# Performance work log

Measured on AMD Instinct MI355X. Metric: run time of the kernel, lower is better.

The kernel has to match this reference:

```python
import jax, jax.numpy as jnp
import numpy as np

B, T, C = 4, 2048, 768
H = 12  # n_head; head_dim = C // H = 64


def setup_inputs() -> dict:
    key = jax.random.key(0)
    k1, k2, k3, k4, k5 = jax.random.split(key, 5)
    scale = 0.02
    return {
        "x": jax.random.normal(k1, (B, T, C), dtype=jnp.float32),
        "w_attn": jax.random.normal(k2, (C, 3 * C), dtype=jnp.float32) * scale,
        "b_attn": jax.random.normal(k3, (3 * C,), dtype=jnp.float32) * scale,
        "w_proj": jax.random.normal(k4, (C, C), dtype=jnp.float32) * scale,
        "b_proj": jax.random.normal(k5, (C,), dtype=jnp.float32) * scale,
    }


def reference(x, w_attn, b_attn, w_proj, b_proj):
    Bx, Tx, Cx = x.shape
    hd = Cx // H  # head dim
    qkv = x @ w_attn + b_attn                       # [B, T, 3C]
    q, k, v = jnp.split(qkv, 3, axis=2)
    # [B, T, H, hd] -> [B, H, T, hd]
    q = q.reshape(Bx, Tx, H, hd).transpose(0, 2, 1, 3)
    k = k.reshape(Bx, Tx, H, hd).transpose(0, 2, 1, 3)
    v = v.reshape(Bx, Tx, H, hd).transpose(0, 2, 1, 3)
    att = jnp.einsum('bhqd,bhkd->bhqk', q, k) / jnp.sqrt(jnp.float32(hd))
    causal = jnp.tril(jnp.ones((Tx, Tx), dtype=bool))
    att = jnp.where(causal[None, None, :, :], att, -jnp.inf)
    att = jax.nn.softmax(att, axis=-1)
    y = jnp.einsum('bhqk,bhkd->bhqd', att, v)       # [B, H, T, hd]
    y = y.transpose(0, 2, 1, 3).reshape(Bx, Tx, Cx)
    return y @ w_proj + b_proj
```

## Files before the change

### kernel.cpp

```cpp
#include <hip/hip_runtime.h>
#include <hip/hip_bf16.h>

using f32x4 = __attribute__((ext_vector_type(4))) float;
using s16x8 = __attribute__((ext_vector_type(8))) short;

#define MFMA16x16x32(a, b, c) __builtin_amdgcn_mfma_f32_16x16x32_bf16((a), (b), (c), 0, 0, 0)

#define AS_G(p) ((const __attribute__((address_space(1))) void*)(p))
#define AS_L(p) ((__attribute__((address_space(3))) void*)(p))

#define BARRIER_LGKM() do { \
    asm volatile("s_waitcnt lgkmcnt(0)" ::: "memory"); \
    __builtin_amdgcn_s_barrier(); \
} while (0)

static __device__ __forceinline__ unsigned short f2bf(float f) {
    unsigned int u = __float_as_uint(f);
    u = (u + 0x7fffu + ((u >> 16) & 1u)) >> 16;
    return (unsigned short)u;
}
static __device__ __forceinline__ unsigned int cvt_pk_bf2(float lo, float hi) {
    unsigned int r;
    asm("v_cvt_pk_bf16_f32 %0, %1, %2" : "=v"(r) : "v"(lo), "v"(hi));
    return r;
}
static __device__ __forceinline__ int swz128(int r, int c) { return (r * 128 + c) ^ ((r & 7) << 4); }

__global__ __launch_bounds__(256)
void prologue_kernel(const float* __restrict__ x, unsigned short* __restrict__ xb,
                     const float* __restrict__ w_attn, unsigned short* __restrict__ wTa,
                     const float* __restrict__ w_proj, unsigned short* __restrict__ wTp) {
    __shared__ float tile[32][33];
    const int bid = blockIdx.x, tid = threadIdx.x;
    if (bid < 2048) {
        const int n = 8192 * 768;
        int i = (bid * 256 + tid) * 4;
        const int stride = 2048 * 256 * 4;
        for (; i < n; i += stride) {
            float4 v = *(const float4*)(x + i);
            ushort4 o;
            o.x = f2bf(v.x); o.y = f2bf(v.y); o.z = f2bf(v.z); o.w = f2bf(v.w);
            *(ushort4*)(xb + i) = o;
        }
    } else {
        const float* w; unsigned short* wt; int K, N, bx, by;
        if (bid < 3776) {
            int id = bid - 2048; w = w_attn; wt = wTa; K = 768; N = 2304;
            bx = id % 72; by = id / 72;
        } else {
            int id = bid - 3776; w = w_proj; wt = wTp; K = 768; N = 768;
            bx = id % 24; by = id / 24;
        }
        const int tx = tid & 31, ty = tid >> 5;
        const int n0 = bx * 32, k0 = by * 32;
#pragma unroll
        for (int r = 0; r < 4; r++)
            tile[ty * 4 + r][tx] = w[(size_t)(k0 + ty * 4 + r) * N + n0 + tx];
        __syncthreads();
#pragma unroll
        for (int r = 0; r < 4; r++)
            wt[(size_t)(n0 + ty * 4 + r) * K + k0 + tx] = f2bf(tile[tx][ty * 4 + r]);
    }
}

template <bool OUT_BF16>
__global__ __launch_bounds__(256, 3)
void gemm_bt64(const unsigned short* __restrict__ A, const unsigned short* __restrict__ Bt,
               const float* __restrict__ bias, void* __restrict__ Cout,
               unsigned short* __restrict__ Vt,
               int M, int N, int K, int ldc, int qcols, float qscale) {
    __shared__ char smem[49152];
    const int tid = threadIdx.x, wid = tid >> 6, lane = tid & 63;
    const int g = lane >> 4, lr = lane & 15;
    const int nx = N >> 7;
    const int ypx = (M >> 6) >> 3;
    const int xcd = blockIdx.x & 7, ii = blockIdx.x >> 3;
    const int m0 = (xcd * ypx + ii / nx) * 64;
    const int n0 = (ii % nx) * 128;

    f32x4 acc[4][2];
#pragma unroll
    for (int i = 0; i < 4; i++)
#pragma unroll
        for (int j = 0; j < 2; j++) acc[i][j] = f32x4{0.f, 0.f, 0.f, 0.f};

    const int rbase = lane >> 3;
    const int cSw = ((lane & 7) << 4) ^ (rbase << 4);

    auto STAGE = [&](int buf, int kt) {
        char* base = smem + buf * 24576;
#pragma unroll
        for (int ww = 0; ww < 2; ww++) {
            int w = wid * 2 + ww;
            int r = w * 8 + rbase;
            const unsigned short* srcA = A + (size_t)(m0 + r) * K + kt + (cSw >> 1);
            __builtin_amdgcn_global_load_lds(AS_G(srcA), AS_L(base + w * 1024), 16, 0, 0);
        }
#pragma unroll
        for (int ww = 0; ww < 4; ww++) {
            int w = wid * 4 + ww;
            int r = w * 8 + rbase;
            const unsigned short* srcB = Bt + (size_t)(n0 + r) * K + kt + (cSw >> 1);
            __builtin_amdgcn_global_load_lds(AS_G(srcB), AS_L(base + 8192 + w * 1024), 16, 0, 0);
        }
    };

    const int nk = K >> 6;
    STAGE(0, 0);

    for (int t = 0; t < nk; t++) {
        if (t + 1 < nk) {
            STAGE((t + 1) & 1, (t + 1) << 6);
            asm volatile("s_waitcnt vmcnt(6)" ::: "memory");
        } else {
            asm volatile("s_waitcnt vmcnt(0)" ::: "memory");
        }
        __builtin_amdgcn_s_barrier();
        char* cbase = smem + (t & 1) * 24576;
#pragma unroll
        for (int ks = 0; ks < 2; ks++) {
            s16x8 af[4], bfr[2];
#pragma unroll
            for (int i = 0; i < 4; i++)
                af[i] = *(const s16x8*)(cbase + swz128(i * 16 + lr, ks * 64 + g * 16));
#pragma unroll
            for (int j = 0; j < 2; j++)
                bfr[j] = *(const s16x8*)(cbase + 8192 + swz128(wid * 32 + j * 16 + lr, ks * 64 + g * 16));
#pragma unroll
            for (int i = 0; i < 4; i++)
#pragma unroll
                for (int j = 0; j < 2; j++)
                    acc[i][j] = MFMA16x16x32(af[i], bfr[j], acc[i][j]);
        }
        BARRIER_LGKM();
    }

    if (Vt != nullptr && n0 >= 1536) {
#pragma unroll
        for (int j = 0; j < 2; j++) {
            int dl = wid * 32 + j * 16 + lr;
            float bv = bias[n0 + dl];
#pragma unroll
            for (int i = 0; i < 4; i++) {
                int tl = i * 16 + g * 4;
                ushort4 o4;
                o4.x = f2bf(acc[i][j][0] + bv);
                o4.y = f2bf(acc[i][j][1] + bv);
                o4.z = f2bf(acc[i][j][2] + bv);
                o4.w = f2bf(acc[i][j][3] + bv);
                *(ushort4*)(smem + swz128(dl, tl * 2)) = o4;
            }
        }
        __syncthreads();
        const int bb = m0 >> 11, t0 = m0 & 2047;
#pragma unroll
        for (int it = 0; it < 4; it++) {
            int dl = it * 32 + (tid >> 3);
            int dg = (n0 - 1536) + dl;
            int hh = dg >> 6, dd = dg & 63;
            s16x8 v = *(const s16x8*)(smem + swz128(dl, (tid & 7) * 16));
            *(s16x8*)(Vt + ((((size_t)bb * 12 + hh) * 64 + dd) << 11) + t0 + (tid & 7) * 8) = v;
        }
    } else {
#pragma unroll
        for (int j = 0; j < 2; j++) {
            int c = n0 + wid * 32 + j * 16 + lr;
            float bv = bias[c];
            float cscale = (c < qcols) ? qscale : 1.0f;
#pragma unroll
            for (int i = 0; i < 4; i++) {
#pragma unroll
                for (int rg = 0; rg < 4; rg++) {
                    int r = m0 + i * 16 + g * 4 + rg;
                    float val = (acc[i][j][rg] + bv) * cscale;
                    if constexpr (OUT_BF16)
                        ((unsigned short*)Cout)[(size_t)r * ldc + c] = f2bf(val);
                    else
                        ((float*)Cout)[(size_t)r * ldc + c] = val;
                }
            }
        }
    }
}

__global__ __launch_bounds__(256, 2)
void attn_kernel(const unsigned short* __restrict__ qk, const unsigned short* __restrict__ Vt,
                 unsigned short* __restrict__ y) {
    __shared__ char smem[49152];
    const int tid = threadIdx.x, wid = tid >> 6, lane = tid & 63;
    const int g = lane >> 4, lr = lane & 15;
    const int T = 2048;

    const int s = blockIdx.x;
    const int xcd = s & 7, i = s >> 3;
    const int grp = xcd * 6 + (i >> 4);
    const int qpi = i & 15;
    const int h = grp % 12, b = grp / 12;
    const int qtA = qpi, qtB = 31 - qpi;
    const int q0A = qtA * 64, q0B = qtB * 64;

    s16x8 vone;
#pragma unroll
    for (int e = 0; e < 8; e++) vone[e] = (short)0x3F80;

    const unsigned short* qrowA = qk + (size_t)(b * T + q0A + wid * 16 + lr) * 1536 + h * 64;
    const unsigned short* qrowB = qk + (size_t)(b * T + q0B + wid * 16 + lr) * 1536 + h * 64;
    s16x8 aqA[2], aqB[2];
    aqA[0] = *(const s16x8*)(qrowA + g * 8);
    aqA[1] = *(const s16x8*)(qrowA + 32 + g * 8);
    aqB[0] = *(const s16x8*)(qrowB + g * 8);
    aqB[1] = *(const s16x8*)(qrowB + 32 + g * 8);

    f32x4 oA[4], oB[4], lsumA, lsumB;
#pragma unroll
    for (int r = 0; r < 4; r++) { oA[r] = f32x4{0.f, 0.f, 0.f, 0.f}; oB[r] = f32x4{0.f, 0.f, 0.f, 0.f}; }
    lsumA = f32x4{0.f, 0.f, 0.f, 0.f};
    lsumB = f32x4{0.f, 0.f, 0.f, 0.f};

    const int rbase = lane >> 3;
    const int cSw = ((lane & 7) << 4) ^ (rbase << 4);
    const unsigned short* pkBase = qk + (size_t)(b * T) * 1536 + 768 + h * 64 + (cSw >> 1);
    const unsigned short* pvBase = Vt + (((size_t)b * 12 + h) << 17) + (cSw >> 1);

    auto STAGE = [&](int buf, int j0) {
        char* kb = smem + buf * 8192;
        char* vb = smem + 16384 + buf * 8192;
#pragma unroll
        for (int ww = 0; ww < 2; ww++) {
            int w = wid * 2 + ww;
            int jj = w * 8 + rbase;
            const unsigned short* srcK = pkBase + (size_t)(j0 + jj) * 1536;
            __builtin_amdgcn_global_load_lds(AS_G(srcK), AS_L(kb + w * 1024), 16, 0, 0);
            const unsigned short* srcV = pvBase + ((size_t)jj << 11) + j0;
            __builtin_amdgcn_global_load_lds(AS_G(srcV), AS_L(vb + w * 1024), 16, 0, 0);
        }
    };

    const int ntA = qtA + 1, ntB = qtB + 1;

    STAGE(0, 0);

    char* const pbaseB = smem + 32768 + wid * 2048;
    char* const pbaseA = smem + 40960 + wid * 2048;
    const int q_rel = wid * 16 + lr;

    for (int t = 0; t < ntB; t++) {
        asm volatile("s_waitcnt vmcnt(0)" ::: "memory");
        BARRIER_LGKM();
        if (t + 1 < ntB) STAGE((t + 1) & 1, (t + 1) * 64);

        char* kbase = smem + (t & 1) * 8192;
        char* vbase = smem + 16384 + (t & 1) * 8192;
        const bool actA = (t < ntA);

        {
            f32x4 st[4];
            __builtin_amdgcn_s_setprio(1);
#pragma unroll
            for (int nf = 0; nf < 4; nf++) {
                f32x4 sf = f32x4{0.f, 0.f, 0.f, 0.f};
#pragma unroll
                for (int ks = 0; ks < 2; ks++) {
                    s16x8 ak = *(const s16x8*)(kbase + swz128(nf * 16 + lr, (ks * 32 + g * 8) * 2));
                    sf = MFMA16x16x32(ak, aqB[ks], sf);
                }
                st[nf] = sf;
            }
            __builtin_amdgcn_s_setprio(0);
            const bool diag = (t == ntB - 1);
#pragma unroll
            for (int nf = 0; nf < 4; nf++)
#pragma unroll
                for (int rg = 0; rg < 4; rg++) {
                    float p = __builtin_amdgcn_exp2f(st[nf][rg]);
                    if (diag && (nf * 16 + g * 4 + rg > q_rel)) p = 0.f;
                    st[nf][rg] = p;
                }
#pragma unroll
            for (int nf = 0; nf < 4; nf++) {
                uint2 dw;
                dw.x = cvt_pk_bf2(st[nf][0], st[nf][1]);
                dw.y = cvt_pk_bf2(st[nf][2], st[nf][3]);
                *(uint2*)(pbaseB + swz128(lr, nf * 32 + g * 8)) = dw;
            }
        }
        if (actA) {
            f32x4 st[4];
            __builtin_amdgcn_s_setprio(1);
#pragma unroll
            for (int nf = 0; nf < 4; nf++) {
                f32x4 sf = f32x4{0.f, 0.f, 0.f, 0.f};
#pragma unroll
                for (int ks = 0; ks < 2; ks++) {
                    s16x8 ak = *(const s16x8*)(kbase + swz128(nf * 16 + lr, (ks * 32 + g * 8) * 2));
                    sf = MFMA16x16x32(ak, aqA[ks], sf);
                }
                st[nf] = sf;
            }
            __builtin_amdgcn_s_setprio(0);
            const bool diag = (t == ntA - 1);
#pragma unroll
            for (int nf = 0; nf < 4; nf++)
#pragma unroll
                for (int rg = 0; rg < 4; rg++) {
                    float p = __builtin_amdgcn_exp2f(st[nf][rg]);
                    if (diag && (nf * 16 + g * 4 + rg > q_rel)) p = 0.f;
                    st[nf][rg] = p;
                }
#pragma unroll
            for (int nf = 0; nf < 4; nf++) {
                uint2 dw;
                dw.x = cvt_pk_bf2(st[nf][0], st[nf][1]);
                dw.y = cvt_pk_bf2(st[nf][2], st[nf][3]);
                *(uint2*)(pbaseA + swz128(lr, nf * 32 + g * 8)) = dw;
            }
        }

        {
            s16x8 pf[2];
#pragma unroll
            for (int ks = 0; ks < 2; ks++)
                pf[ks] = *(const s16x8*)(pbaseB + swz128(lr, ks * 64 + g * 16));
            __builtin_amdgcn_s_setprio(1);
#pragma unroll
            for (int nf = 0; nf < 4; nf++) {
#pragma unroll
                for (int ks = 0; ks < 2; ks++) {
                    s16x8 bv = *(const s16x8*)(vbase + swz128(nf * 16 + lr, ks * 64 + g * 16));
                    oB[nf] = MFMA16x16x32(pf[ks], bv, oB[nf]);
                }
            }
            lsumB = MFMA16x16x32(pf[0], vone, lsumB);
            lsumB = MFMA16x16x32(pf[1], vone, lsumB);
            __builtin_amdgcn_s_setprio(0);
        }
        if (actA) {
            s16x8 pf[2];
#pragma unroll
            for (int ks = 0; ks < 2; ks++)
                pf[ks] = *(const s16x8*)(pbaseA + swz128(lr, ks * 64 + g * 16));
            __builtin_amdgcn_s_setprio(1);
#pragma unroll
            for (int nf = 0; nf < 4; nf++) {
#pragma unroll
                for (int ks = 0; ks < 2; ks++) {
                    s16x8 bv = *(const s16x8*)(vbase + swz128(nf * 16 + lr, ks * 64 + g * 16));
                    oA[nf] = MFMA16x16x32(pf[ks], bv, oA[nf]);
                }
            }
            lsumA = MFMA16x16x32(pf[0], vone, lsumA);
            lsumA = MFMA16x16x32(pf[1], vone, lsumA);
            __builtin_amdgcn_s_setprio(0);
        }
    }

#pragma unroll
    for (int which = 0; which < 2; which++) {
        const f32x4 lsum = which ? lsumB : lsumA;
        const int q0 = which ? q0B : q0A;
        f32x4* o = which ? oB : oA;
        float linv_q[4];
#pragma unroll
        for (int rg = 0; rg < 4; rg++) linv_q[rg] = 1.0f / lsum[rg];
#pragma unroll
        for (int nf = 0; nf < 4; nf++) {
#pragma unroll
            for (int rg = 0; rg < 4; rg++) {
                int row = b * T + q0 + wid * 16 + g * 4 + rg;
                int col = h * 64 + nf * 16 + lr;
                y[(size_t)row * 768 + col] = f2bf(o[nf][rg] * linv_q[rg]);
            }
        }
    }
}

extern "C" void kernel_launch(void* const* d_in, const int* in_sizes, int n_in,
                              void* d_out, int out_size, void* d_ws, size_t ws_size,
                              hipStream_t stream) {
    const float* x      = (const float*)d_in[0];
    const float* w_attn = (const float*)d_in[1];
    const float* b_attn = (const float*)d_in[2];
    const float* w_proj = (const float*)d_in[3];
    const float* b_proj = (const float*)d_in[4];

    char* ws = (char*)d_ws;
    unsigned short* qk  = (unsigned short*)(ws);
    unsigned short* Vt  = (unsigned short*)(ws + 25165824);
    unsigned short* wTa = (unsigned short*)(ws + 37748736);
    unsigned short* wTp = (unsigned short*)(ws + 41287680);

    const bool big = ws_size >= (size_t)55050240;
    unsigned short* xb = (unsigned short*)d_out;
    unsigned short* yb = big ? (unsigned short*)(ws + 42467328)
                             : (unsigned short*)((char*)d_out + 12582912);
    float* projOut = big ? (float*)d_out : (float*)ws;

    prologue_kernel<<<4352, 256, 0, stream>>>(x, xb, w_attn, wTa, w_proj, wTp);

    gemm_bt64<true><<<2304, 256, 0, stream>>>(xb, wTa, b_attn, (void*)qk, Vt,
                                              8192, 2304, 768, 1536, 768, 0.1803368801111244f);
    attn_kernel<<<768, 256, 0, stream>>>(qk, Vt, yb);
    gemm_bt64<false><<<768, 256, 0, stream>>>(yb, wTp, b_proj, (void*)projOut, nullptr,
                                              8192, 768, 768, 768, 0, 1.0f);
    if (!big)
        hipMemcpyAsync(d_out, projOut, 25165824, hipMemcpyDeviceToDevice, stream);
}
```

Before: 115.4 us.

## Process paired query tiles sequentially instead of sharing K/V tiles

The attention kernel stops processing its two causal query tiles (qpi and 31-qpi) together over one shared K/V stream. It now runs them one after another, each with its own K/V staging loop, which frees one P buffer and cuts LDS from 48KB to 40KB. The cost is that K/V tiles for the shorter range are loaded twice, and a barrier separates the two passes. Barriers also drop the explicit lgkmcnt(0) wait, which relies on the compiler's own waitcnt insertion for LDS reads.

```diff
diff --git a/kernel.cpp b/kernel.cpp
--- a/kernel.cpp
+++ b/kernel.cpp
@@ -8,11 +8,6 @@
 
 #define AS_G(p) ((const __attribute__((address_space(1))) void*)(p))
 #define AS_L(p) ((__attribute__((address_space(3))) void*)(p))
-
-#define BARRIER_LGKM() do { \
-    asm volatile("s_waitcnt lgkmcnt(0)" ::: "memory"); \
-    __builtin_amdgcn_s_barrier(); \
-} while (0)
 
 static __device__ __forceinline__ unsigned short f2bf(float f) {
     unsigned int u = __float_as_uint(f);
@@ -132,7 +127,7 @@
                 for (int j = 0; j < 2; j++)
                     acc[i][j] = MFMA16x16x32(af[i], bfr[j], acc[i][j]);
         }
-        BARRIER_LGKM();
+        __builtin_amdgcn_s_barrier();
     }
 
     if (Vt != nullptr && n0 >= 1536) {
@@ -186,7 +181,7 @@
 __global__ __launch_bounds__(256, 2)
 void attn_kernel(const unsigned short* __restrict__ qk, const unsigned short* __restrict__ Vt,
                  unsigned short* __restrict__ y) {
-    __shared__ char smem[49152];
+    __shared__ char smem[40960];
     const int tid = threadIdx.x, wid = tid >> 6, lane = tid & 63;
     const int g = lane >> 4, lr = lane & 15;
     const int T = 2048;
@@ -196,26 +191,10 @@
     const int grp = xcd * 6 + (i >> 4);
     const int qpi = i & 15;
     const int h = grp % 12, b = grp / 12;
-    const int qtA = qpi, qtB = 31 - qpi;
-    const int q0A = qtA * 64, q0B = qtB * 64;
 
     s16x8 vone;
 #pragma unroll
     for (int e = 0; e < 8; e++) vone[e] = (short)0x3F80;
-
-    const unsigned short* qrowA = qk + (size_t)(b * T + q0A + wid * 16 + lr) * 1536 + h * 64;
-    const unsigned short* qrowB = qk + (size_t)(b * T + q0B + wid * 16 + lr) * 1536 + h * 64;
-    s16x8 aqA[2], aqB[2];
-    aqA[0] = *(const s16x8*)(qrowA + g * 8);
-    aqA[1] = *(const s16x8*)(qrowA + 32 + g * 8);
-    aqB[0] = *(const s16x8*)(qrowB + g * 8);
-    aqB[1] = *(const s16x8*)(qrowB + 32 + g * 8);
-
-    f32x4 oA[4], oB[4], lsumA, lsumB;
-#pragma unroll
-    for (int r = 0; r < 4; r++) { oA[r] = f32x4{0.f, 0.f, 0.f, 0.f}; oB[r] = f32x4{0.f, 0.f, 0.f, 0.f}; }
-    lsumA = f32x4{0.f, 0.f, 0.f, 0.f};
-    lsumB = f32x4{0.f, 0.f, 0.f, 0.f};
 
     const int rbase = lane >> 3;
     const int cSw = ((lane & 7) << 4) ^ (rbase << 4);
@@ -236,24 +215,35 @@
         }
     };
 
-    const int ntA = qtA + 1, ntB = qtB + 1;
-
-    STAGE(0, 0);
-
-    char* const pbaseB = smem + 32768 + wid * 2048;
-    char* const pbaseA = smem + 40960 + wid * 2048;
+    char* const pbase = smem + 32768 + wid * 2048;
     const int q_rel = wid * 16 + lr;
 
-    for (int t = 0; t < ntB; t++) {
-        asm volatile("s_waitcnt vmcnt(0)" ::: "memory");
-        BARRIER_LGKM();
-        if (t + 1 < ntB) STAGE((t + 1) & 1, (t + 1) * 64);
-
-        char* kbase = smem + (t & 1) * 8192;
-        char* vbase = smem + 16384 + (t & 1) * 8192;
-        const bool actA = (t < ntA);
-
-        {
+    for (int pp = 0; pp < 2; pp++) {
+        const int qt = pp ? (31 - qpi) : qpi;
+        const int q0 = qt * 64;
+        const int nt = qt + 1;
+
+        const unsigned short* qrow = qk + (size_t)(b * T + q0 + wid * 16 + lr) * 1536 + h * 64;
+        s16x8 aq[2];
+        aq[0] = *(const s16x8*)(qrow + g * 8);
+        aq[1] = *(const s16x8*)(qrow + 32 + g * 8);
+
+        f32x4 o[4], lsum;
+#pragma unroll
+        for (int r = 0; r < 4; r++) o[r] = f32x4{0.f, 0.f, 0.f, 0.f};
+        lsum = f32x4{0.f, 0.f, 0.f, 0.f};
+
+        if (pp) __builtin_amdgcn_s_barrier();
+        STAGE(0, 0);
+
+        for (int t = 0; t < nt; t++) {
+            asm volatile("s_waitcnt vmcnt(0)" ::: "memory");
+            __builtin_amdgcn_s_barrier();
+            if (t + 1 < nt) STAGE((t + 1) & 1, (t + 1) * 64);
+
+            char* kbase = smem + (t & 1) * 8192;
+            char* vbase = smem + 16384 + (t & 1) * 8192;
+
             f32x4 st[4];
             __builtin_amdgcn_s_setprio(1);
 #pragma unroll
@@ -262,12 +252,13 @@
 #pragma unroll
                 for (int ks = 0; ks < 2; ks++) {
                     s16x8 ak = *(const s16x8*)(kbase + swz128(nf * 16 + lr, (ks * 32 + g * 8) * 2));
-                    sf = MFMA16x16x32(ak, aqB[ks], sf);
+                    sf = MFMA16x16x32(ak, aq[ks], sf);
                 }
                 st[nf] = sf;
             }
             __builtin_amdgcn_s_setprio(0);
-            const bool diag = (t == ntB - 1);
+
+            const bool diag = (t == nt - 1);
 #pragma unroll
             for (int nf = 0; nf < 4; nf++)
 #pragma unroll
@@ -281,84 +272,27 @@
                 uint2 dw;
                 dw.x = cvt_pk_bf2(st[nf][0], st[nf][1]);
                 dw.y = cvt_pk_bf2(st[nf][2], st[nf][3]);
-                *(uint2*)(pbaseB + swz128(lr, nf * 32 + g * 8)) = dw;
-            }
-        }
-        if (actA) {
-            f32x4 st[4];
-            __builtin_amdgcn_s_setprio(1);
-#pragma unroll
-            for (int nf = 0; nf < 4; nf++) {
-                f32x4 sf = f32x4{0.f, 0.f, 0.f, 0.f};
-#pragma unroll
-                for (int ks = 0; ks < 2; ks++) {
-                    s16x8 ak = *(const s16x8*)(kbase + swz128(nf * 16 + lr, (ks * 32 + g * 8) * 2));
-                    sf = MFMA16x16x32(ak, aqA[ks], sf);
-                }
-                st[nf] = sf;
-            }
-            __builtin_amdgcn_s_setprio(0);
-            const bool diag = (t == ntA - 1);
-#pragma unroll
-            for (int nf = 0; nf < 4; nf++)
-#pragma unroll
-                for (int rg = 0; rg < 4; rg++) {
-                    float p = __builtin_amdgcn_exp2f(st[nf][rg]);
-                    if (diag && (nf * 16 + g * 4 + rg > q_rel)) p = 0.f;
-                    st[nf][rg] = p;
-                }
-#pragma unroll
-            for (int nf = 0; nf < 4; nf++) {
-                uint2 dw;
-                dw.x = cvt_pk_bf2(st[nf][0], st[nf][1]);
-                dw.y = cvt_pk_bf2(st[nf][2], st[nf][3]);
-                *(uint2*)(pbaseA + swz128(lr, nf * 32 + g * 8)) = dw;
-            }
-        }
-
-        {
+                *(uint2*)(pbase + swz128(lr, nf * 32 + g * 8)) = dw;
+            }
+
             s16x8 pf[2];
 #pragma unroll
             for (int ks = 0; ks < 2; ks++)
-                pf[ks] = *(const s16x8*)(pbaseB + swz128(lr, ks * 64 + g * 16));
+                pf[ks] = *(const s16x8*)(pbase + swz128(lr, ks * 64 + g * 16));
             __builtin_amdgcn_s_setprio(1);
 #pragma unroll
             for (int nf = 0; nf < 4; nf++) {
 #pragma unroll
                 for (int ks = 0; ks < 2; ks++) {
                     s16x8 bv = *(const s16x8*)(vbase + swz128(nf * 16 + lr, ks * 64 + g * 16));
-                    oB[nf] = MFMA16x16x32(pf[ks], bv, oB[nf]);
+                    o[nf] = MFMA16x16x32(pf[ks], bv, o[nf]);
                 }
             }
-            lsumB = MFMA16x16x32(pf[0], vone, lsumB);
-            lsumB = MFMA16x16x32(pf[1], vone, lsumB);
+            lsum = MFMA16x16x32(pf[0], vone, lsum);
+            lsum = MFMA16x16x32(pf[1], vone, lsum);
             __builtin_amdgcn_s_setprio(0);
         }
-        if (actA) {
-            s16x8 pf[2];
-#pragma unroll
-            for (int ks = 0; ks < 2; ks++)
-                pf[ks] = *(const s16x8*)(pbaseA + swz128(lr, ks * 64 + g * 16));
-            __builtin_amdgcn_s_setprio(1);
-#pragma unroll
-            for (int nf = 0; nf < 4; nf++) {
-#pragma unroll
-                for (int ks = 0; ks < 2; ks++) {
-                    s16x8 bv = *(const s16x8*)(vbase + swz128(nf * 16 + lr, ks * 64 + g * 16));
-                    oA[nf] = MFMA16x16x32(pf[ks], bv, oA[nf]);
-                }
-            }
-            lsumA = MFMA16x16x32(pf[0], vone, lsumA);
-            lsumA = MFMA16x16x32(pf[1], vone, lsumA);
-            __builtin_amdgcn_s_setprio(0);
-        }
-    }
-
-#pragma unroll
-    for (int which = 0; which < 2; which++) {
-        const f32x4 lsum = which ? lsumB : lsumA;
-        const int q0 = which ? q0B : q0A;
-        f32x4* o = which ? oB : oA;
+
         float linv_q[4];
 #pragma unroll
         for (int rg = 0; rg < 4; rg++) linv_q[rg] = 1.0f / lsum[rg];
```

Result: no change. 114.8 us (-0.5%).
